# Optimization experiments

Hardware: AMD Instinct MI355X
Metric: run time of the kernel (lower is better)

Reference implementation:

```python
import jax, jax.numpy as jnp
import numpy as np

NODE_DIM = 128
CAT = 16
N_NODES = 100000
N_EDGES = 200000
N_SCALARS = 6
INPUT_DIM = 5 * NODE_DIM + 5 * CAT + N_SCALARS  # 726
CELL_H, NET_H, OUT = 192, 128, 128
EPS = 1e-5


def setup_inputs() -> dict:
    key = jax.random.key(0)
    ks = jax.random.split(key, 24)
    inp = {
        'h_nodes': jax.random.normal(ks[0], (N_NODES, NODE_DIM), jnp.float32),
        'edge_scalars': jax.random.normal(ks[1], (N_EDGES, N_SCALARS), jnp.float32),
        'edge_src': jax.random.randint(ks[2], (N_EDGES,), 0, N_NODES),
        'edge_dst': jax.random.randint(ks[3], (N_EDGES,), 0, N_NODES),
        'edge_type': jax.random.randint(ks[4], (N_EDGES,), 0, 2),
        'cell_type_src': jax.random.randint(ks[5], (N_EDGES,), 0, 256),
        'cell_type_dst': jax.random.randint(ks[6], (N_EDGES,), 0, 256),
        'pin_role_src': jax.random.randint(ks[7], (N_EDGES,), 0, 64),
        'pin_role_dst': jax.random.randint(ks[8], (N_EDGES,), 0, 64),
        # embedding tables
        'emb_edge_type': jax.random.normal(ks[9], (2, CAT), jnp.float32),
        'emb_cell_type': jax.random.normal(ks[10], (256, CAT), jnp.float32),
        'emb_pin_role': jax.random.normal(ks[11], (64, CAT), jnp.float32),
        # cell MLP params
        'cell_W1': jax.random.normal(ks[12], (INPUT_DIM, CELL_H), jnp.float32) * (1.0 / np.sqrt(INPUT_DIM)),
        'cell_b1': jnp.zeros((CELL_H,), jnp.float32),
        'cell_g': jnp.ones((CELL_H,), jnp.float32),
        'cell_beta': jnp.zeros((CELL_H,), jnp.float32),
        'cell_W2': jax.random.normal(ks[13], (CELL_H, OUT), jnp.float32) * (1.0 / np.sqrt(CELL_H)),
        'cell_b2': jnp.zeros((OUT,), jnp.float32),
        # net MLP params
        'net_W1': jax.random.normal(ks[14], (INPUT_DIM, NET_H), jnp.float32) * (1.0 / np.sqrt(INPUT_DIM)),
        'net_b1': jnp.zeros((NET_H,), jnp.float32),
        'net_g': jnp.ones((NET_H,), jnp.float32),
        'net_beta': jnp.zeros((NET_H,), jnp.float32),
        'net_W2': jax.random.normal(ks[15], (NET_H, OUT), jnp.float32) * (1.0 / np.sqrt(NET_H)),
        'net_b2': jnp.zeros((OUT,), jnp.float32),
    }
    return inp


def _oov(x, n):
    return jnp.where((x >= 0) & (x < n), x, 0)


def _mlp(x, W1, b1, g, beta, W2, b2):
    h = x @ W1 + b1
    mu = jnp.mean(h, axis=-1, keepdims=True)
    var = jnp.mean(jnp.square(h - mu), axis=-1, keepdims=True)
    h = (h - mu) * jax.lax.rsqrt(var + EPS) * g + beta
    h = jax.nn.relu(h)
    return h @ W2 + b2


def reference(h_nodes, edge_scalars, emb_edge_type, emb_cell_type, emb_pin_role,
              cell_W1, cell_b1, cell_g, cell_beta, cell_W2, cell_b2,
              net_W1, net_b1, net_g, net_beta, net_W2, net_b2,
              edge_src, edge_dst, edge_type, cell_type_src, cell_type_dst,
              pin_role_src, pin_role_dst):
    h_u = h_nodes[edge_src]                      # [E, D]
    h_v = h_nodes[edge_dst]
    h_prod = h_u * h_v
    h_abs_diff = jnp.abs(h_u - h_v)
    h_signed_diff = h_v - h_u
    e_et = emb_edge_type[_oov(edge_type, emb_edge_type.shape[0])]
    e_ct_s = emb_cell_type[_oov(cell_type_src, emb_cell_type.shape[0])]
    e_ct_d = emb_cell_type[_oov(cell_type_dst, emb_cell_type.shape[0])]
    e_pr_s = emb_pin_role[_oov(pin_role_src, emb_pin_role.shape[0])]
    e_pr_d = emb_pin_role[_oov(pin_role_dst, emb_pin_role.shape[0])]
    scal = jnp.clip(edge_scalars, -10.0, 10.0)
    feat = jnp.concatenate([h_u, h_v, h_prod, h_abs_diff, h_signed_diff,
                            e_et, e_ct_s, e_ct_d, e_pr_s, e_pr_d, scal], axis=-1)  # [E, 726]
    out_cell = _mlp(feat, cell_W1, cell_b1, cell_g, cell_beta, cell_W2, cell_b2)
    out_net = _mlp(feat, net_W1, net_b1, net_g, net_beta, net_W2, net_b2)
    et = edge_type[:, None]
    h_edges = jnp.where(et == 0, out_cell, jnp.where(et == 1, out_net, jnp.zeros_like(out_cell)))
    return h_edges
```

## Files before the change

kernel.cpp:

```cpp
#include <hip/hip_runtime.h>

#define KS 23

typedef short bfrag8 __attribute__((ext_vector_type(8)));
typedef float f32x4 __attribute__((ext_vector_type(4)));

__device__ __forceinline__ unsigned short f2bf(float f) {
  union { float f; unsigned u; } v; v.f = f;
  unsigned r = v.u + 0x7fffu + ((v.u >> 16) & 1u);
  return (unsigned short)(r >> 16);
}
__device__ __forceinline__ unsigned pk2(float a, float b) {
  return (unsigned)f2bf(a) | ((unsigned)f2bf(b) << 16);
}
__device__ __forceinline__ float bf2f(short s) {
  union { unsigned u; float f; } v;
  v.u = ((unsigned)(unsigned short)s) << 16;
  return v.f;
}

__global__ void prep_weights(const float* __restrict__ cW1, const float* __restrict__ nW1,
                             const float* __restrict__ cW2, const float* __restrict__ nW2,
                             unsigned short* __restrict__ w1c, unsigned short* __restrict__ w1n,
                             unsigned short* __restrict__ w2c, unsigned short* __restrict__ w2n,
                             int* __restrict__ cnt) {
  int i = blockIdx.x * blockDim.x + threadIdx.x;
  if (i == 0) { cnt[0] = 0; cnt[1] = 0; }
  const int T0 = 12 * KS * 512, T1 = 8 * KS * 512, T2 = 8 * 6 * 512, T3 = 8 * 4 * 512;
  const int tot = T0 + T1 + T2 + T3;
  for (; i < tot; i += gridDim.x * blockDim.x) {
    int idx = i;
    const float* src; unsigned short* dst; int N, Kreal, KSm, rel;
    if (idx < T0)              { src = cW1; dst = w1c; N = 192; Kreal = 726; KSm = KS; rel = idx; }
    else if ((idx -= T0) < T1) { src = nW1; dst = w1n; N = 128; Kreal = 726; KSm = KS; rel = idx; }
    else if ((idx -= T1) < T2) { src = cW2; dst = w2c; N = 128; Kreal = 192; KSm = 6;  rel = idx; }
    else { idx -= T2;            src = nW2; dst = w2n; N = 128; Kreal = 128; KSm = 4;  rel = idx; }
    int blk = rel >> 9, within = rel & 511;
    int l = within >> 3, e = within & 7;
    int n16 = blk / KSm, k32 = blk - n16 * KSm;
    int n = n16 * 16 + (l & 15);
    int k = k32 * 32 + ((l >> 4) * 8) + e;
    dst[rel] = f2bf(k < Kreal ? src[(size_t)k * N + n] : 0.f);
  }
}

__global__ void compact_edges(const int* __restrict__ et,
                              const int* __restrict__ esrc, const int* __restrict__ edst,
                              const int* __restrict__ cts, const int* __restrict__ ctd,
                              const int* __restrict__ prs, const int* __restrict__ prd,
                              int* __restrict__ cnt, int4* __restrict__ r0, int4* __restrict__ r1,
                              float* __restrict__ out, int n) {
  int i = blockIdx.x * blockDim.x + threadIdx.x;
  for (; i < n; i += gridDim.x * blockDim.x) {
    int ty = et[i];
    if (ty == 0 || ty == 1) {
      int c1 = cts[i]; c1 = ((unsigned)c1 < 256u) ? c1 : 0;
      int c2 = ctd[i]; c2 = ((unsigned)c2 < 256u) ? c2 : 0;
      int p1 = prs[i]; p1 = ((unsigned)p1 < 64u)  ? p1 : 0;
      int p2 = prd[i]; p2 = ((unsigned)p2 < 64u)  ? p2 : 0;
      int4 rec; rec.x = esrc[i]; rec.y = edst[i]; rec.z = i;
      rec.w = c1 | (c2 << 8) | (p1 << 16) | (p2 << 22);
      if (ty == 0) r0[atomicAdd(&cnt[0], 1)] = rec;
      else         r1[atomicAdd(&cnt[1], 1)] = rec;
    } else {
      float4 z = make_float4(0.f, 0.f, 0.f, 0.f);
      float4* po = (float4*)(out + (size_t)i * 128);
      #pragma unroll
      for (int j = 0; j < 32; ++j) po[j] = z;
    }
  }
}

__device__ __forceinline__ void loadrow(const float* __restrict__ p, int kq, bfrag8 f[4]) {
  #pragma unroll
  for (int j = 0; j < 4; ++j) {
    float4 x = *(const float4*)(p + j * 32 + kq);
    float4 y = *(const float4*)(p + j * 32 + kq + 4);
    union { bfrag8 b; uint4 q; } r;
    r.q = make_uint4(pk2(x.x, x.y), pk2(x.z, x.w), pk2(y.x, y.y), pk2(y.z, y.w));
    f[j] = r.b;
  }
}

__device__ __forceinline__ bfrag8 dfrag(bfrag8 u, bfrag8 v, int op) {
  unsigned w[4];
  #pragma unroll
  for (int i = 0; i < 4; ++i) {
    float u0 = bf2f(u[2 * i]),     v0 = bf2f(v[2 * i]);
    float u1 = bf2f(u[2 * i + 1]), v1 = bf2f(v[2 * i + 1]);
    float x0 = (op == 0) ? u0 * v0 : (op == 1) ? fabsf(u0 - v0) : v0 - u0;
    float x1 = (op == 0) ? u1 * v1 : (op == 1) ? fabsf(u1 - v1) : v1 - u1;
    w[i] = pk2(x0, x1);
  }
  union { bfrag8 b; uint4 q; } r;
  r.q = make_uint4(w[0], w[1], w[2], w[3]);
  return r.b;
}

template <int CH>
__device__ __forceinline__ void mlp_tile2(
    char* smraw, int lane, int ni, int tile, int c, int etv,
    const int4* __restrict__ rec,
    const float* __restrict__ h_nodes, const float* __restrict__ edge_scalars,
    const float* __restrict__ emb_et, const float* __restrict__ emb_ct, const float* __restrict__ emb_pr,
    const unsigned short* __restrict__ w1f, const unsigned short* __restrict__ w2f,
    const float* __restrict__ b1, const float* __restrict__ g,
    const float* __restrict__ beta, const float* __restrict__ b2,
    float* __restrict__ out)
{
  constexpr int NF  = CH / 32;
  constexpr int KS2 = CH / 32;
  constexpr int HST = CH + 8;
  constexpr int EST = 104;
  unsigned short (*emb)[EST] = (unsigned short (*)[EST])(smraw + ni * 6656);
  unsigned short (*hb)[HST]  = (unsigned short (*)[HST])smraw;
  float (*red)[32][2] = (float (*)[32][2])(smraw + 13312);

  const int lrow = lane & 15;
  const int grp  = lane >> 4;
  const int kq   = grp * 8;
  const int base = tile * 32;

  int4 qa = rec[min(base + lrow, c - 1)];
  int4 qb = rec[min(base + 16 + lrow, c - 1)];

  {
    const int rr = lane >> 1, hf = lane & 1;
    int4 qe = rec[min(base + rr, c - 1)];
    const int pk = qe.w;
    if (hf == 0) {
      const float* tps[3] = { emb_et + etv * 16,
                              emb_ct + (pk & 255) * 16,
                              emb_ct + ((pk >> 8) & 255) * 16 };
      #pragma unroll
      for (int tb = 0; tb < 3; ++tb) {
        const float4* tp = (const float4*)tps[tb];
        float4 a = tp[0], b4 = tp[1], c4 = tp[2], d4 = tp[3];
        *(uint4*)&emb[rr][tb * 16 + 0] =
          make_uint4(pk2(a.x, a.y), pk2(a.z, a.w), pk2(b4.x, b4.y), pk2(b4.z, b4.w));
        *(uint4*)&emb[rr][tb * 16 + 8] =
          make_uint4(pk2(c4.x, c4.y), pk2(c4.z, c4.w), pk2(d4.x, d4.y), pk2(d4.z, d4.w));
      }
    } else {
      const float* tps[2] = { emb_pr + ((pk >> 16) & 63) * 16,
                              emb_pr + ((pk >> 22) & 63) * 16 };
      #pragma unroll
      for (int tb = 0; tb < 2; ++tb) {
        const float4* tp = (const float4*)tps[tb];
        float4 a = tp[0], b4 = tp[1], c4 = tp[2], d4 = tp[3];
        *(uint4*)&emb[rr][48 + tb * 16 + 0] =
          make_uint4(pk2(a.x, a.y), pk2(a.z, a.w), pk2(b4.x, b4.y), pk2(b4.z, b4.w));
        *(uint4*)&emb[rr][48 + tb * 16 + 8] =
          make_uint4(pk2(c4.x, c4.y), pk2(c4.z, c4.w), pk2(d4.x, d4.y), pk2(d4.z, d4.w));
      }
      const float2* sp = (const float2*)(edge_scalars + (size_t)qe.z * 6);
      float2 s0 = sp[0], s1 = sp[1], s2 = sp[2];
      float v0 = fminf(fmaxf(s0.x, -10.f), 10.f), v1 = fminf(fmaxf(s0.y, -10.f), 10.f);
      float v2 = fminf(fmaxf(s1.x, -10.f), 10.f), v3 = fminf(fmaxf(s1.y, -10.f), 10.f);
      float v4 = fminf(fmaxf(s2.x, -10.f), 10.f), v5 = fminf(fmaxf(s2.y, -10.f), 10.f);
      *(uint4*)&emb[rr][80] = make_uint4(pk2(v0, v1), pk2(v2, v3), pk2(v4, v5), 0u);
      *(uint4*)&emb[rr][88] = make_uint4(0u, 0u, 0u, 0u);
    }
  }

  bfrag8 ua[4], va[4], ub[4], vb[4];
  loadrow(h_nodes + (size_t)qa.x * 128, kq, ua);
  loadrow(h_nodes + (size_t)qa.y * 128, kq, va);
  loadrow(h_nodes + (size_t)qb.x * 128, kq, ub);
  loadrow(h_nodes + (size_t)qb.y * 128, kq, vb);

  f32x4 acc1[2][NF];
  #pragma unroll
  for (int mf = 0; mf < 2; ++mf)
    #pragma unroll
    for (int nf = 0; nf < NF; ++nf) acc1[mf][nf] = 0;
  const unsigned short* wbl = w1f + ((size_t)ni * NF * KS) * 512 + (size_t)lane * 8;

  bfrag8 br[2][NF];
  #pragma unroll
  for (int nf = 0; nf < NF; ++nf)
    br[0][nf] = *(const bfrag8*)(wbl + ((size_t)nf * KS) * 512);
  #pragma unroll
  for (int kk = 0; kk < 23; ++kk) {
    if (kk + 1 < 23) {
      #pragma unroll
      for (int nf = 0; nf < NF; ++nf)
        br[(kk + 1) & 1][nf] = *(const bfrag8*)(wbl + ((size_t)nf * KS + kk + 1) * 512);
    }
    bfrag8 a0, a1;
    const int seg = kk >> 2, k = kk & 3;
    if (kk >= 20) {
      a0 = *(const bfrag8*)&emb[lrow][(kk - 20) * 32 + kq];
      a1 = *(const bfrag8*)&emb[16 + lrow][(kk - 20) * 32 + kq];
    } else if (seg == 0) { a0 = ua[k]; a1 = ub[k]; }
    else if (seg == 1)   { a0 = va[k]; a1 = vb[k]; }
    else { a0 = dfrag(ua[k], va[k], seg - 2); a1 = dfrag(ub[k], vb[k], seg - 2); }
    #pragma unroll
    for (int nf = 0; nf < NF; ++nf) {
      acc1[0][nf] = __builtin_amdgcn_mfma_f32_16x16x32_bf16(a0, br[kk & 1][nf], acc1[0][nf], 0, 0, 0);
      acc1[1][nf] = __builtin_amdgcn_mfma_f32_16x16x32_bf16(a1, br[kk & 1][nf], acc1[1][nf], 0, 0, 0);
    }
  }

  float b1r[NF], gr[NF], ber[NF];
  #pragma unroll
  for (int nf = 0; nf < NF; ++nf) {
    int n = ni * (CH / 2) + nf * 16 + lrow;
    b1r[nf] = b1[n]; gr[nf] = g[n]; ber[nf] = beta[n];
  }
  float sums[2][4], sqs[2][4];
  #pragma unroll
  for (int mf = 0; mf < 2; ++mf)
    #pragma unroll
    for (int rg = 0; rg < 4; ++rg) {
      float s = 0.f, qd = 0.f;
      #pragma unroll
      for (int nf = 0; nf < NF; ++nf) {
        float v = acc1[mf][nf][rg] + b1r[nf];
        acc1[mf][nf][rg] = v;
        s += v; qd += v * v;
      }
      sums[mf][rg] = s; sqs[mf][rg] = qd;
    }
  #pragma unroll
  for (int d = 1; d < 16; d <<= 1) {
    #pragma unroll
    for (int mf = 0; mf < 2; ++mf)
      #pragma unroll
      for (int rg = 0; rg < 4; ++rg) {
        sums[mf][rg] += __shfl_xor(sums[mf][rg], d);
        sqs[mf][rg]  += __shfl_xor(sqs[mf][rg], d);
      }
  }
  if (lrow == 0) {
    #pragma unroll
    for (int mf = 0; mf < 2; ++mf)
      #pragma unroll
      for (int rg = 0; rg < 4; ++rg) {
        int row = mf * 16 + grp * 4 + rg;
        red[ni][row][0] = sums[mf][rg];
        red[ni][row][1] = sqs[mf][rg];
      }
  }
  __syncthreads();

  #pragma unroll
  for (int mf = 0; mf < 2; ++mf)
    #pragma unroll
    for (int rg = 0; rg < 4; ++rg) {
      int row = mf * 16 + grp * 4 + rg;
      float ss = red[0][row][0] + red[1][row][0];
      float qq = red[0][row][1] + red[1][row][1];
      float mu = ss * (1.f / CH);
      float var = fmaxf(qq * (1.f / CH) - mu * mu, 0.f);
      float rs = rsqrtf(var + 1e-5f);
      #pragma unroll
      for (int nf = 0; nf < NF; ++nf) {
        float v = (acc1[mf][nf][rg] - mu) * rs * gr[nf] + ber[nf];
        hb[row][ni * (CH / 2) + nf * 16 + lrow] = f2bf(fmaxf(v, 0.f));
      }
    }
  __syncthreads();

  float b2r[4];
  #pragma unroll
  for (int nf2 = 0; nf2 < 4; ++nf2) b2r[nf2] = b2[ni * 64 + nf2 * 16 + lrow];

  f32x4 acc2[2][4];
  #pragma unroll
  for (int mf = 0; mf < 2; ++mf)
    #pragma unroll
    for (int nf2 = 0; nf2 < 4; ++nf2) acc2[mf][nf2] = 0;
  const unsigned short* wbl2 = w2f + (size_t)lane * 8;
  bfrag8 cr[2][4];
  #pragma unroll
  for (int nf2 = 0; nf2 < 4; ++nf2)
    cr[0][nf2] = *(const bfrag8*)(wbl2 + ((size_t)(ni * 4 + nf2) * KS2) * 512);
  #pragma unroll
  for (int k2 = 0; k2 < KS2; ++k2) {
    if (k2 + 1 < KS2) {
      #pragma unroll
      for (int nf2 = 0; nf2 < 4; ++nf2)
        cr[(k2 + 1) & 1][nf2] = *(const bfrag8*)(wbl2 + ((size_t)(ni * 4 + nf2) * KS2 + k2 + 1) * 512);
    }
    bfrag8 a0 = *(const bfrag8*)&hb[lrow][k2 * 32 + kq];
    bfrag8 a1 = *(const bfrag8*)&hb[16 + lrow][k2 * 32 + kq];
    #pragma unroll
    for (int nf2 = 0; nf2 < 4; ++nf2) {
      acc2[0][nf2] = __builtin_amdgcn_mfma_f32_16x16x32_bf16(a0, cr[k2 & 1][nf2], acc2[0][nf2], 0, 0, 0);
      acc2[1][nf2] = __builtin_amdgcn_mfma_f32_16x16x32_bf16(a1, cr[k2 & 1][nf2], acc2[1][nf2], 0, 0, 0);
    }
  }

  #pragma unroll
  for (int mf = 0; mf < 2; ++mf)
    #pragma unroll
    for (int rg = 0; rg < 4; ++rg) {
      const int rowLow = grp * 4 + rg;
      const int eid = __shfl(mf ? qb.z : qa.z, rowLow);
      if (base + mf * 16 + rowLow < c) {
        float* po = out + (size_t)eid * 128 + ni * 64 + lrow;
        #pragma unroll
        for (int nf2 = 0; nf2 < 4; ++nf2)
          po[nf2 * 16] = acc2[mf][nf2][rg] + b2r[nf2];
      }
    }
}

struct Args {
  const float *h_nodes, *edge_scalars;
  const float *emb_et, *emb_ct, *emb_pr;
  const unsigned short *w1c, *w2c;
  const float *cb1, *cg, *cbe, *cb2;
  const unsigned short *w1n, *w2n;
  const float *nb1, *ng, *nbe, *nb2;
  const int *cnt;
  const int4 *r0, *r1;
  float* out;
};

__global__ __launch_bounds__(128, 2) void edge_mlp_all(Args A) {
  __shared__ alignas(16) char smraw[13312 + 512];
  const int lane = threadIdx.x & 63;
  const int ni   = threadIdx.x >> 6;
  const int b = blockIdx.x;
  const int c0 = A.cnt[0];
  const int t0 = (c0 + 31) >> 5;
  if (b < t0) {
    mlp_tile2<192>(smraw, lane, ni, b, c0, 0, A.r0, A.h_nodes, A.edge_scalars,
                   A.emb_et, A.emb_ct, A.emb_pr, A.w1c, A.w2c,
                   A.cb1, A.cg, A.cbe, A.cb2, A.out);
  } else {
    const int c1 = A.cnt[1];
    const int t2 = b - t0;
    if (t2 * 32 < c1)
      mlp_tile2<128>(smraw, lane, ni, t2, c1, 1, A.r1, A.h_nodes, A.edge_scalars,
                     A.emb_et, A.emb_ct, A.emb_pr, A.w1n, A.w2n,
                     A.nb1, A.ng, A.nbe, A.nb2, A.out);
  }
}

extern "C" void kernel_launch(void* const* d_in, const int* in_sizes, int n_in,
                              void* d_out, int out_size, void* d_ws, size_t ws_size,
                              hipStream_t stream) {
  (void)n_in; (void)out_size; (void)ws_size;
  const float* h_nodes      = (const float*)d_in[0];
  const float* edge_scalars = (const float*)d_in[1];
  const int*   edge_src     = (const int*)d_in[2];
  const int*   edge_dst     = (const int*)d_in[3];
  const int*   edge_type    = (const int*)d_in[4];
  const int*   ct_s         = (const int*)d_in[5];
  const int*   ct_d         = (const int*)d_in[6];
  const int*   pr_s         = (const int*)d_in[7];
  const int*   pr_d         = (const int*)d_in[8];
  const float* emb_et       = (const float*)d_in[9];
  const float* emb_ct       = (const float*)d_in[10];
  const float* emb_pr       = (const float*)d_in[11];
  const float* cW1 = (const float*)d_in[12];
  const float* cb1 = (const float*)d_in[13];
  const float* cg  = (const float*)d_in[14];
  const float* cbe = (const float*)d_in[15];
  const float* cW2 = (const float*)d_in[16];
  const float* cb2 = (const float*)d_in[17];
  const float* nW1 = (const float*)d_in[18];
  const float* nb1 = (const float*)d_in[19];
  const float* ng  = (const float*)d_in[20];
  const float* nbe = (const float*)d_in[21];
  const float* nW2 = (const float*)d_in[22];
  const float* nb2 = (const float*)d_in[23];
  const int n_edges = in_sizes[2];
  float* out = (float*)d_out;

  char* ws = (char*)d_ws;
  int* cnt = (int*)ws;
  int4* r0 = (int4*)(ws + 256);
  int4* r1 = r0 + n_edges;
  size_t woff = (256 + (size_t)2 * n_edges * sizeof(int4) + 255) & ~(size_t)255;
  unsigned short* w1c = (unsigned short*)(ws + woff);
  unsigned short* w1n = w1c + 12 * KS * 512;
  unsigned short* w2c = w1n + 8 * KS * 512;
  unsigned short* w2n = w2c + 8 * 6 * 512;

  prep_weights<<<1080, 256, 0, stream>>>(cW1, nW1, cW2, nW2, w1c, w1n, w2c, w2n, cnt);
  compact_edges<<<(n_edges + 255) / 256, 256, 0, stream>>>(edge_type, edge_src, edge_dst,
                                                           ct_s, ct_d, pr_s, pr_d,
                                                           cnt, r0, r1, out, n_edges);

  Args A;
  A.h_nodes = h_nodes; A.edge_scalars = edge_scalars;
  A.emb_et = emb_et; A.emb_ct = emb_ct; A.emb_pr = emb_pr;
  A.w1c = w1c; A.w2c = w2c; A.cb1 = cb1; A.cg = cg; A.cbe = cbe; A.cb2 = cb2;
  A.w1n = w1n; A.w2n = w2n; A.nb1 = nb1; A.ng = ng; A.nbe = nbe; A.nb2 = nb2;
  A.cnt = cnt; A.r0 = r0; A.r1 = r1; A.out = out;

  const int tiles = (n_edges + 31) / 32 + 2;
  edge_mlp_all<<<tiles, 128, 0, stream>>>(A);
}
```

Baseline: 259.5 us.

## Stream W1 fragments through a 3-deep LDS ring via global_load_lds

Replaces the register double-buffered global loads of W1 weight fragments with a 3-slot ring in shared memory, filled by direct global-to-LDS async loads and guarded by explicit vmcnt waits. The intent is to keep more weight loads in flight and free VGPRs, hiding global latency behind the MFMA loop. In exchange it grows the block's LDS footprint to about 50KB, which can limit occupancy. It also relies on hand-counted waitcnt values that must match the compiler's instruction stream, and adds an LDS read per fragment.

```diff
diff --git a/kernel.cpp b/kernel.cpp
--- a/kernel.cpp
+++ b/kernel.cpp
@@ -1,6 +1,7 @@
 #include <hip/hip_runtime.h>
 
 #define KS 23
+#define RING 3
 
 typedef short bfrag8 __attribute__((ext_vector_type(8)));
 typedef float f32x4 __attribute__((ext_vector_type(4)));
@@ -17,6 +18,11 @@
   union { unsigned u; float f; } v;
   v.u = ((unsigned)(unsigned short)s) << 16;
   return v.f;
+}
+__device__ __forceinline__ void gload_lds16(const void* g, void* l) {
+  __builtin_amdgcn_global_load_lds(
+      (const __attribute__((address_space(1))) void*)g,
+      (__attribute__((address_space(3))) void*)l, 16, 0, 0);
 }
 
 __global__ void prep_weights(const float* __restrict__ cW1, const float* __restrict__ nW1,
@@ -112,9 +118,11 @@
   constexpr int KS2 = CH / 32;
   constexpr int HST = CH + 8;
   constexpr int EST = 104;
-  unsigned short (*emb)[EST] = (unsigned short (*)[EST])(smraw + ni * 6656);
+  constexpr int RB  = RING * NF * 1024;
+  unsigned short* ring = (unsigned short*)(smraw + ni * RB);
+  unsigned short (*emb)[EST] = (unsigned short (*)[EST])(smraw + 2 * RB + ni * 6656);
   unsigned short (*hb)[HST]  = (unsigned short (*)[HST])smraw;
-  float (*red)[32][2] = (float (*)[32][2])(smraw + 13312);
+  float (*red)[32][2] = (float (*)[32][2])(smraw + 2 * RB + 13312);
 
   const int lrow = lane & 15;
   const int grp  = lane >> 4;
@@ -169,23 +177,33 @@
   loadrow(h_nodes + (size_t)qb.x * 128, kq, ub);
   loadrow(h_nodes + (size_t)qb.y * 128, kq, vb);
 
+  auto stage = [&](int kk) {
+    const int slot = kk % RING;
+    #pragma unroll
+    for (int nf = 0; nf < NF; ++nf) {
+      const unsigned short* gp = w1f + (((size_t)(ni * NF + nf)) * KS + kk) * 512 + lane * 8;
+      unsigned short* lp = ring + (slot * NF + nf) * 512;
+      gload_lds16(gp, lp);
+    }
+  };
+  stage(0); stage(1); stage(2);
+
   f32x4 acc1[2][NF];
   #pragma unroll
   for (int mf = 0; mf < 2; ++mf)
     #pragma unroll
     for (int nf = 0; nf < NF; ++nf) acc1[mf][nf] = 0;
-  const unsigned short* wbl = w1f + ((size_t)ni * NF * KS) * 512 + (size_t)lane * 8;
-
-  bfrag8 br[2][NF];
-  #pragma unroll
-  for (int nf = 0; nf < NF; ++nf)
-    br[0][nf] = *(const bfrag8*)(wbl + ((size_t)nf * KS) * 512);
+
   #pragma unroll
   for (int kk = 0; kk < 23; ++kk) {
-    if (kk + 1 < 23) {
-      #pragma unroll
-      for (int nf = 0; nf < NF; ++nf)
-        br[(kk + 1) & 1][nf] = *(const bfrag8*)(wbl + ((size_t)nf * KS + kk + 1) * 512);
+    if (kk < 21) {
+      if constexpr (NF == 6) asm volatile("s_waitcnt vmcnt(12)" ::: "memory");
+      else                   asm volatile("s_waitcnt vmcnt(8)"  ::: "memory");
+    } else if (kk == 21) {
+      if constexpr (NF == 6) asm volatile("s_waitcnt vmcnt(6)" ::: "memory");
+      else                   asm volatile("s_waitcnt vmcnt(4)" ::: "memory");
+    } else {
+      asm volatile("s_waitcnt vmcnt(0)" ::: "memory");
     }
     bfrag8 a0, a1;
     const int seg = kk >> 2, k = kk & 3;
@@ -195,10 +213,16 @@
     } else if (seg == 0) { a0 = ua[k]; a1 = ub[k]; }
     else if (seg == 1)   { a0 = va[k]; a1 = vb[k]; }
     else { a0 = dfrag(ua[k], va[k], seg - 2); a1 = dfrag(ub[k], vb[k], seg - 2); }
+    const int slot = kk % RING;
     #pragma unroll
     for (int nf = 0; nf < NF; ++nf) {
-      acc1[0][nf] = __builtin_amdgcn_mfma_f32_16x16x32_bf16(a0, br[kk & 1][nf], acc1[0][nf], 0, 0, 0);
-      acc1[1][nf] = __builtin_amdgcn_mfma_f32_16x16x32_bf16(a1, br[kk & 1][nf], acc1[1][nf], 0, 0, 0);
+      bfrag8 bf = *(const bfrag8*)(ring + (slot * NF + nf) * 512 + lane * 8);
+      acc1[0][nf] = __builtin_amdgcn_mfma_f32_16x16x32_bf16(a0, bf, acc1[0][nf], 0, 0, 0);
+      acc1[1][nf] = __builtin_amdgcn_mfma_f32_16x16x32_bf16(a1, bf, acc1[1][nf], 0, 0, 0);
+    }
+    if (kk + RING < 23) {
+      asm volatile("s_waitcnt lgkmcnt(0)" ::: "memory");
+      stage(kk + RING);
     }
   }
 
@@ -320,7 +344,7 @@
 };
 
 __global__ __launch_bounds__(128, 2) void edge_mlp_all(Args A) {
-  __shared__ alignas(16) char smraw[13312 + 512];
+  __shared__ alignas(16) char smraw[50688];
   const int lane = threadIdx.x & 63;
   const int ni   = threadIdx.x >> 6;
   const int b = blockIdx.x;
```

Result: faster. 243.1 us (-6.3%).

## Enlarge edge tile to 128 rows with LDS-staged shared weights

Applied to the files above, without the earlier changes.

Restructures the fused edge MLP from 32-edge tiles on 2 waves into 128-edge tiles on 8 waves, a 4x2 wave grid over rows and output columns. W1 fragments are staged once per block into double-buffered LDS through global_load_lds. Feature fragments (u, v, product and diffs) are built cooperatively into LDS, so each weight load is amortised over four times as many edges. This adds a block-wide barrier per K step, uses about 74KB of LDS per block, and lowers the number of blocks, which may cut occupancy. It also switches bf16 conversion to the library intrinsic.

```diff
diff --git a/kernel.cpp b/kernel.cpp
--- a/kernel.cpp
+++ b/kernel.cpp
@@ -1,22 +1,29 @@
 #include <hip/hip_runtime.h>
+#include <hip/hip_bf16.h>
 
 #define KS 23
+#define BM 128
 
 typedef short bfrag8 __attribute__((ext_vector_type(8)));
 typedef float f32x4 __attribute__((ext_vector_type(4)));
 
 __device__ __forceinline__ unsigned short f2bf(float f) {
-  union { float f; unsigned u; } v; v.f = f;
-  unsigned r = v.u + 0x7fffu + ((v.u >> 16) & 1u);
-  return (unsigned short)(r >> 16);
+  union { __hip_bfloat16 h; unsigned short s; } v;
+  v.h = __float2bfloat16(f);
+  return v.s;
 }
 __device__ __forceinline__ unsigned pk2(float a, float b) {
   return (unsigned)f2bf(a) | ((unsigned)f2bf(b) << 16);
 }
-__device__ __forceinline__ float bf2f(short s) {
+__device__ __forceinline__ float bf2f(unsigned short s) {
   union { unsigned u; float f; } v;
-  v.u = ((unsigned)(unsigned short)s) << 16;
+  v.u = ((unsigned)s) << 16;
   return v.f;
+}
+__device__ __forceinline__ void gload_lds16(const void* g, void* l) {
+  __builtin_amdgcn_global_load_lds(
+      (const __attribute__((address_space(1))) void*)g,
+      (__attribute__((address_space(3))) void*)l, 16, 0, 0);
 }
 
 __global__ void prep_weights(const float* __restrict__ cW1, const float* __restrict__ nW1,
@@ -71,35 +78,9 @@
   }
 }
 
-__device__ __forceinline__ void loadrow(const float* __restrict__ p, int kq, bfrag8 f[4]) {
-  #pragma unroll
-  for (int j = 0; j < 4; ++j) {
-    float4 x = *(const float4*)(p + j * 32 + kq);
-    float4 y = *(const float4*)(p + j * 32 + kq + 4);
-    union { bfrag8 b; uint4 q; } r;
-    r.q = make_uint4(pk2(x.x, x.y), pk2(x.z, x.w), pk2(y.x, y.y), pk2(y.z, y.w));
-    f[j] = r.b;
-  }
-}
-
-__device__ __forceinline__ bfrag8 dfrag(bfrag8 u, bfrag8 v, int op) {
-  unsigned w[4];
-  #pragma unroll
-  for (int i = 0; i < 4; ++i) {
-    float u0 = bf2f(u[2 * i]),     v0 = bf2f(v[2 * i]);
-    float u1 = bf2f(u[2 * i + 1]), v1 = bf2f(v[2 * i + 1]);
-    float x0 = (op == 0) ? u0 * v0 : (op == 1) ? fabsf(u0 - v0) : v0 - u0;
-    float x1 = (op == 0) ? u1 * v1 : (op == 1) ? fabsf(u1 - v1) : v1 - u1;
-    w[i] = pk2(x0, x1);
-  }
-  union { bfrag8 b; uint4 q; } r;
-  r.q = make_uint4(w[0], w[1], w[2], w[3]);
-  return r.b;
-}
-
 template <int CH>
-__device__ __forceinline__ void mlp_tile2(
-    char* smraw, int lane, int ni, int tile, int c, int etv,
+__device__ __forceinline__ void mlp_tile(
+    char* smraw, int* sEid, int tile, int c, int etv,
     const int4* __restrict__ rec,
     const float* __restrict__ h_nodes, const float* __restrict__ edge_scalars,
     const float* __restrict__ emb_et, const float* __restrict__ emb_ct, const float* __restrict__ emb_pr,
@@ -108,103 +89,141 @@
     const float* __restrict__ beta, const float* __restrict__ b2,
     float* __restrict__ out)
 {
-  constexpr int NF  = CH / 32;
+  constexpr int NFW = CH / 32;
+  constexpr int NT1 = CH / 16;
   constexpr int KS2 = CH / 32;
-  constexpr int HST = CH + 8;
-  constexpr int EST = 104;
-  unsigned short (*emb)[EST] = (unsigned short (*)[EST])(smraw + ni * 6656);
-  unsigned short (*hb)[HST]  = (unsigned short (*)[HST])smraw;
-  float (*red)[32][2] = (float (*)[32][2])(smraw + 13312);
-
+  constexpr int CHP = CH + 8;
+  unsigned short* Bb = (unsigned short*)smraw;
+  unsigned short (*fc)[128][40] = (unsigned short (*)[128][40])(smraw + 24576);
+  unsigned short (*emb)[104]    = (unsigned short (*)[104])(smraw + 45056);
+  float (*red)[128][2]          = (float (*)[128][2])(smraw + 71680);
+  unsigned short (*hb)[CHP]     = (unsigned short (*)[CHP])smraw;
+
+  const int t    = threadIdx.x;
+  const int lane = t & 63;
+  const int wid  = t >> 6;
+  const int mi   = wid & 3;
+  const int ni   = wid >> 2;
   const int lrow = lane & 15;
-  const int grp  = lane >> 4;
-  const int kq   = grp * 8;
-  const int base = tile * 32;
-
-  int4 qa = rec[min(base + lrow, c - 1)];
-  int4 qb = rec[min(base + 16 + lrow, c - 1)];
+  const int kq   = (lane >> 4) * 8;
+  const int r    = t >> 2;
+  const int l4   = t & 3;
+  const int base = tile * BM;
+
+  const int idx = base + r;
+  const bool valid = idx < c;
+  int4 q = rec[min(idx, c - 1)];
+  if (l4 == 0) sEid[r] = valid ? q.z : -1;
+
+  const float* bu = h_nodes + (size_t)q.x * 128;
+  const float* bv = h_nodes + (size_t)q.y * 128;
+  unsigned upk[4][4], vpk[4][4];
+  #pragma unroll
+  for (int j = 0; j < 4; ++j) {
+    float4 a = *(const float4*)(bu + j * 32 + l4 * 8);
+    float4 b = *(const float4*)(bu + j * 32 + l4 * 8 + 4);
+    upk[j][0] = pk2(a.x, a.y); upk[j][1] = pk2(a.z, a.w);
+    upk[j][2] = pk2(b.x, b.y); upk[j][3] = pk2(b.z, b.w);
+    float4 cc = *(const float4*)(bv + j * 32 + l4 * 8);
+    float4 d  = *(const float4*)(bv + j * 32 + l4 * 8 + 4);
+    vpk[j][0] = pk2(cc.x, cc.y); vpk[j][1] = pk2(cc.z, cc.w);
+    vpk[j][2] = pk2(d.x, d.y);   vpk[j][3] = pk2(d.z, d.w);
+  }
 
   {
-    const int rr = lane >> 1, hf = lane & 1;
-    int4 qe = rec[min(base + rr, c - 1)];
-    const int pk = qe.w;
-    if (hf == 0) {
-      const float* tps[3] = { emb_et + etv * 16,
-                              emb_ct + (pk & 255) * 16,
-                              emb_ct + ((pk >> 8) & 255) * 16 };
-      #pragma unroll
-      for (int tb = 0; tb < 3; ++tb) {
-        const float4* tp = (const float4*)tps[tb];
-        float4 a = tp[0], b4 = tp[1], c4 = tp[2], d4 = tp[3];
-        *(uint4*)&emb[rr][tb * 16 + 0] =
-          make_uint4(pk2(a.x, a.y), pk2(a.z, a.w), pk2(b4.x, b4.y), pk2(b4.z, b4.w));
-        *(uint4*)&emb[rr][tb * 16 + 8] =
-          make_uint4(pk2(c4.x, c4.y), pk2(c4.z, c4.w), pk2(d4.x, d4.y), pk2(d4.z, d4.w));
-      }
-    } else {
-      const float* tps[2] = { emb_pr + ((pk >> 16) & 63) * 16,
-                              emb_pr + ((pk >> 22) & 63) * 16 };
-      #pragma unroll
-      for (int tb = 0; tb < 2; ++tb) {
-        const float4* tp = (const float4*)tps[tb];
-        float4 a = tp[0], b4 = tp[1], c4 = tp[2], d4 = tp[3];
-        *(uint4*)&emb[rr][48 + tb * 16 + 0] =
-          make_uint4(pk2(a.x, a.y), pk2(a.z, a.w), pk2(b4.x, b4.y), pk2(b4.z, b4.w));
-        *(uint4*)&emb[rr][48 + tb * 16 + 8] =
-          make_uint4(pk2(c4.x, c4.y), pk2(c4.z, c4.w), pk2(d4.x, d4.y), pk2(d4.z, d4.w));
-      }
-      const float2* sp = (const float2*)(edge_scalars + (size_t)qe.z * 6);
+    const int pk = q.w;
+    auto wemb = [&](int col, const float* tp) {
+      float4 a = ((const float4*)tp)[0], b = ((const float4*)tp)[1];
+      float4 cc = ((const float4*)tp)[2], d = ((const float4*)tp)[3];
+      *(uint4*)&emb[r][col]     = make_uint4(pk2(a.x, a.y), pk2(a.z, a.w), pk2(b.x, b.y), pk2(b.z, b.w));
+      *(uint4*)&emb[r][col + 8] = make_uint4(pk2(cc.x, cc.y), pk2(cc.z, cc.w), pk2(d.x, d.y), pk2(d.z, d.w));
+    };
+    if (l4 == 0) {
+      wemb(0, emb_et + etv * 16);
+      const float2* sp = (const float2*)(edge_scalars + (size_t)q.z * 6);
       float2 s0 = sp[0], s1 = sp[1], s2 = sp[2];
       float v0 = fminf(fmaxf(s0.x, -10.f), 10.f), v1 = fminf(fmaxf(s0.y, -10.f), 10.f);
       float v2 = fminf(fmaxf(s1.x, -10.f), 10.f), v3 = fminf(fmaxf(s1.y, -10.f), 10.f);
       float v4 = fminf(fmaxf(s2.x, -10.f), 10.f), v5 = fminf(fmaxf(s2.y, -10.f), 10.f);
-      *(uint4*)&emb[rr][80] = make_uint4(pk2(v0, v1), pk2(v2, v3), pk2(v4, v5), 0u);
-      *(uint4*)&emb[rr][88] = make_uint4(0u, 0u, 0u, 0u);
-    }
-  }
-
-  bfrag8 ua[4], va[4], ub[4], vb[4];
-  loadrow(h_nodes + (size_t)qa.x * 128, kq, ua);
-  loadrow(h_nodes + (size_t)qa.y * 128, kq, va);
-  loadrow(h_nodes + (size_t)qb.x * 128, kq, ub);
-  loadrow(h_nodes + (size_t)qb.y * 128, kq, vb);
-
-  f32x4 acc1[2][NF];
+      *(uint4*)&emb[r][80] = make_uint4(pk2(v0, v1), pk2(v2, v3), pk2(v4, v5), 0u);
+      *(uint4*)&emb[r][88] = make_uint4(0u, 0u, 0u, 0u);
+    } else if (l4 == 1) {
+      wemb(16, emb_ct + (pk & 255) * 16);
+    } else if (l4 == 2) {
+      wemb(32, emb_ct + ((pk >> 8) & 255) * 16);
+    } else {
+      wemb(48, emb_pr + ((pk >> 16) & 63) * 16);
+      wemb(64, emb_pr + ((pk >> 22) & 63) * 16);
+    }
+  }
+
+  auto stageB = [&](int kk, int buf) {
+    unsigned short* dst = Bb + buf * 6144;
+    const unsigned short* gp = w1f + ((size_t)wid * KS + kk) * 512 + lane * 8;
+    gload_lds16(gp, dst + wid * 512);
+    if (NT1 > 8 && wid < NT1 - 8) {
+      const unsigned short* gp2 = w1f + ((size_t)(wid + 8) * KS + kk) * 512 + lane * 8;
+      gload_lds16(gp2, dst + (wid + 8) * 512);
+    }
+  };
+  auto stageF = [&](int kk, int buf) {
+    const int seg = kk >> 2, j = kk & 3;
+    uint4 w;
+    if (seg == 0)      w = make_uint4(upk[j][0], upk[j][1], upk[j][2], upk[j][3]);
+    else if (seg == 1) w = make_uint4(vpk[j][0], vpk[j][1], vpk[j][2], vpk[j][3]);
+    else {
+      unsigned wo[4];
+      #pragma unroll
+      for (int p = 0; p < 4; ++p) {
+        float u0 = bf2f((unsigned short)(upk[j][p] & 0xffff));
+        float u1 = bf2f((unsigned short)(upk[j][p] >> 16));
+        float v0 = bf2f((unsigned short)(vpk[j][p] & 0xffff));
+        float v1 = bf2f((unsigned short)(vpk[j][p] >> 16));
+        float x0 = (seg == 2) ? u0 * v0 : (seg == 3) ? fabsf(u0 - v0) : v0 - u0;
+        float x1 = (seg == 2) ? u1 * v1 : (seg == 3) ? fabsf(u1 - v1) : v1 - u1;
+        wo[p] = pk2(x0, x1);
+      }
+      w = make_uint4(wo[0], wo[1], wo[2], wo[3]);
+    }
+    *(uint4*)&fc[buf][r][l4 * 8] = w;
+  };
+
+  stageB(0, 0);
+  stageF(0, 0);
+  __syncthreads();
+
+  f32x4 acc1[2][NFW];
   #pragma unroll
   for (int mf = 0; mf < 2; ++mf)
     #pragma unroll
-    for (int nf = 0; nf < NF; ++nf) acc1[mf][nf] = 0;
-  const unsigned short* wbl = w1f + ((size_t)ni * NF * KS) * 512 + (size_t)lane * 8;
-
-  bfrag8 br[2][NF];
-  #pragma unroll
-  for (int nf = 0; nf < NF; ++nf)
-    br[0][nf] = *(const bfrag8*)(wbl + ((size_t)nf * KS) * 512);
+    for (int nf = 0; nf < NFW; ++nf) acc1[mf][nf] = 0;
+
   #pragma unroll
   for (int kk = 0; kk < 23; ++kk) {
-    if (kk + 1 < 23) {
-      #pragma unroll
-      for (int nf = 0; nf < NF; ++nf)
-        br[(kk + 1) & 1][nf] = *(const bfrag8*)(wbl + ((size_t)nf * KS + kk + 1) * 512);
-    }
+    const int buf = kk & 1, nbuf = buf ^ 1;
+    if (kk + 1 < 23) stageB(kk + 1, nbuf);
+    if (kk + 1 < 20) stageF(kk + 1, nbuf);
     bfrag8 a0, a1;
-    const int seg = kk >> 2, k = kk & 3;
-    if (kk >= 20) {
-      a0 = *(const bfrag8*)&emb[lrow][(kk - 20) * 32 + kq];
-      a1 = *(const bfrag8*)&emb[16 + lrow][(kk - 20) * 32 + kq];
-    } else if (seg == 0) { a0 = ua[k]; a1 = ub[k]; }
-    else if (seg == 1)   { a0 = va[k]; a1 = vb[k]; }
-    else { a0 = dfrag(ua[k], va[k], seg - 2); a1 = dfrag(ub[k], vb[k], seg - 2); }
-    #pragma unroll
-    for (int nf = 0; nf < NF; ++nf) {
-      acc1[0][nf] = __builtin_amdgcn_mfma_f32_16x16x32_bf16(a0, br[kk & 1][nf], acc1[0][nf], 0, 0, 0);
-      acc1[1][nf] = __builtin_amdgcn_mfma_f32_16x16x32_bf16(a1, br[kk & 1][nf], acc1[1][nf], 0, 0, 0);
-    }
-  }
-
-  float b1r[NF], gr[NF], ber[NF];
-  #pragma unroll
-  for (int nf = 0; nf < NF; ++nf) {
+    if (kk < 20) {
+      a0 = *(const bfrag8*)&fc[buf][mi * 16 + lrow][kq];
+      a1 = *(const bfrag8*)&fc[buf][64 + mi * 16 + lrow][kq];
+    } else {
+      a0 = *(const bfrag8*)&emb[mi * 16 + lrow][(kk - 20) * 32 + kq];
+      a1 = *(const bfrag8*)&emb[64 + mi * 16 + lrow][(kk - 20) * 32 + kq];
+    }
+    const unsigned short* bp = Bb + buf * 6144 + (ni * NFW) * 512 + lane * 8;
+    #pragma unroll
+    for (int nf = 0; nf < NFW; ++nf) {
+      bfrag8 bf = *(const bfrag8*)(bp + nf * 512);
+      acc1[0][nf] = __builtin_amdgcn_mfma_f32_16x16x32_bf16(a0, bf, acc1[0][nf], 0, 0, 0);
+      acc1[1][nf] = __builtin_amdgcn_mfma_f32_16x16x32_bf16(a1, bf, acc1[1][nf], 0, 0, 0);
+    }
+    __syncthreads();
+  }
+
+  float b1r[NFW], gr[NFW], ber[NFW];
+  #pragma unroll
+  for (int nf = 0; nf < NFW; ++nf) {
     int n = ni * (CH / 2) + nf * 16 + lrow;
     b1r[nf] = b1[n]; gr[nf] = g[n]; ber[nf] = beta[n];
   }
@@ -215,7 +234,7 @@
     for (int rg = 0; rg < 4; ++rg) {
       float s = 0.f, qd = 0.f;
       #pragma unroll
-      for (int nf = 0; nf < NF; ++nf) {
+      for (int nf = 0; nf < NFW; ++nf) {
         float v = acc1[mf][nf][rg] + b1r[nf];
         acc1[mf][nf][rg] = v;
         s += v; qd += v * v;
@@ -233,11 +252,12 @@
       }
   }
   if (lrow == 0) {
+    const int grp = lane >> 4;
     #pragma unroll
     for (int mf = 0; mf < 2; ++mf)
       #pragma unroll
       for (int rg = 0; rg < 4; ++rg) {
-        int row = mf * 16 + grp * 4 + rg;
+        int row = mf * 64 + mi * 16 + grp * 4 + rg;
         red[ni][row][0] = sums[mf][rg];
         red[ni][row][1] = sqs[mf][rg];
       }
@@ -248,14 +268,14 @@
   for (int mf = 0; mf < 2; ++mf)
     #pragma unroll
     for (int rg = 0; rg < 4; ++rg) {
-      int row = mf * 16 + grp * 4 + rg;
+      int row = mf * 64 + mi * 16 + (lane >> 4) * 4 + rg;
       float ss = red[0][row][0] + red[1][row][0];
       float qq = red[0][row][1] + red[1][row][1];
       float mu = ss * (1.f / CH);
       float var = fmaxf(qq * (1.f / CH) - mu * mu, 0.f);
       float rs = rsqrtf(var + 1e-5f);
       #pragma unroll
-      for (int nf = 0; nf < NF; ++nf) {
+      for (int nf = 0; nf < NFW; ++nf) {
         float v = (acc1[mf][nf][rg] - mu) * rs * gr[nf] + ber[nf];
         hb[row][ni * (CH / 2) + nf * 16 + lrow] = f2bf(fmaxf(v, 0.f));
       }
@@ -265,7 +285,6 @@
   float b2r[4];
   #pragma unroll
   for (int nf2 = 0; nf2 < 4; ++nf2) b2r[nf2] = b2[ni * 64 + nf2 * 16 + lrow];
-
   f32x4 acc2[2][4];
   #pragma unroll
   for (int mf = 0; mf < 2; ++mf)
@@ -283,8 +302,8 @@
       for (int nf2 = 0; nf2 < 4; ++nf2)
         cr[(k2 + 1) & 1][nf2] = *(const bfrag8*)(wbl2 + ((size_t)(ni * 4 + nf2) * KS2 + k2 + 1) * 512);
     }
-    bfrag8 a0 = *(const bfrag8*)&hb[lrow][k2 * 32 + kq];
-    bfrag8 a1 = *(const bfrag8*)&hb[16 + lrow][k2 * 32 + kq];
+    bfrag8 a0 = *(const bfrag8*)&hb[mi * 16 + lrow][k2 * 32 + kq];
+    bfrag8 a1 = *(const bfrag8*)&hb[64 + mi * 16 + lrow][k2 * 32 + kq];
     #pragma unroll
     for (int nf2 = 0; nf2 < 4; ++nf2) {
       acc2[0][nf2] = __builtin_amdgcn_mfma_f32_16x16x32_bf16(a0, cr[k2 & 1][nf2], acc2[0][nf2], 0, 0, 0);
@@ -296,9 +315,9 @@
   for (int mf = 0; mf < 2; ++mf)
     #pragma unroll
     for (int rg = 0; rg < 4; ++rg) {
-      const int rowLow = grp * 4 + rg;
-      const int eid = __shfl(mf ? qb.z : qa.z, rowLow);
-      if (base + mf * 16 + rowLow < c) {
+      int row = mf * 64 + mi * 16 + (lane >> 4) * 4 + rg;
+      int eid = sEid[row];
+      if (eid >= 0) {
         float* po = out + (size_t)eid * 128 + ni * 64 + lrow;
         #pragma unroll
         for (int nf2 = 0; nf2 < 4; ++nf2)
@@ -319,24 +338,23 @@
   float* out;
 };
 
-__global__ __launch_bounds__(128, 2) void edge_mlp_all(Args A) {
-  __shared__ alignas(16) char smraw[13312 + 512];
-  const int lane = threadIdx.x & 63;
-  const int ni   = threadIdx.x >> 6;
+__global__ __launch_bounds__(512, 4) void edge_mlp_all(Args A) {
+  __shared__ alignas(16) char smraw[73728];
+  __shared__ int sEid[BM];
+  const int c0 = A.cnt[0];
+  const int t0 = (c0 + BM - 1) / BM;
   const int b = blockIdx.x;
-  const int c0 = A.cnt[0];
-  const int t0 = (c0 + 31) >> 5;
   if (b < t0) {
-    mlp_tile2<192>(smraw, lane, ni, b, c0, 0, A.r0, A.h_nodes, A.edge_scalars,
-                   A.emb_et, A.emb_ct, A.emb_pr, A.w1c, A.w2c,
-                   A.cb1, A.cg, A.cbe, A.cb2, A.out);
+    mlp_tile<192>(smraw, sEid, b, c0, 0, A.r0, A.h_nodes, A.edge_scalars,
+                  A.emb_et, A.emb_ct, A.emb_pr, A.w1c, A.w2c,
+                  A.cb1, A.cg, A.cbe, A.cb2, A.out);
   } else {
     const int c1 = A.cnt[1];
     const int t2 = b - t0;
-    if (t2 * 32 < c1)
-      mlp_tile2<128>(smraw, lane, ni, t2, c1, 1, A.r1, A.h_nodes, A.edge_scalars,
-                     A.emb_et, A.emb_ct, A.emb_pr, A.w1n, A.w2n,
-                     A.nb1, A.ng, A.nbe, A.nb2, A.out);
+    if (t2 * BM < c1)
+      mlp_tile<128>(smraw, sEid, t2, c1, 1, A.r1, A.h_nodes, A.edge_scalars,
+                    A.emb_et, A.emb_ct, A.emb_pr, A.w1n, A.w2n,
+                    A.nb1, A.ng, A.nbe, A.nb2, A.out);
   }
 }
 
@@ -393,6 +411,6 @@
   A.w1n = w1n; A.w2n = w2n; A.nb1 = nb1; A.ng = ng; A.nbe = nbe; A.nb2 = nb2;
   A.cnt = cnt; A.r0 = r0; A.r1 = r1; A.out = out;
 
-  const int tiles = (n_edges + 31) / 32 + 2;
-  edge_mlp_all<<<tiles, 128, 0, stream>>>(A);
-}
+  const int nbAll = (n_edges + BM - 1) / BM + 2;
+  edge_mlp_all<<<nbAll, 512, 0, stream>>>(A);
+}
```

After: 227.4 us. 12.4% less time.
